# Optimization experiments

Hardware: AMD Instinct MI355X
Metric: run time of the kernel (lower is better)

The kernel has to match this reference:

```python
import jax, jax.numpy as jnp
import numpy as np

B, C, Himg, Wimg = 4, 256, 64, 64
HID = 256
K = 8
EPS_NORM = 1e-12
BN_EPS = 1e-5


def setup_inputs() -> dict:
    key = jax.random.key(0)
    ks = jax.random.split(key, 14)
    s = lambda fan: 1.0 / np.sqrt(fan)
    inp = {
        "features": jax.random.normal(ks[0], (B, C, Himg, Wimg), dtype=jnp.float32),
        # HypergraphConv 0: theta (C->HID), phi (HID->HID). Weights stored [in,out].
        "theta0_w": jax.random.normal(ks[1], (C, HID), dtype=jnp.float32) * s(C),
        "theta0_b": jnp.zeros((HID,), jnp.float32),
        "phi0_w": jax.random.normal(ks[2], (HID, HID), dtype=jnp.float32) * s(HID),
        "phi0_b": jnp.zeros((HID,), jnp.float32),
        # HypergraphConv 1: theta (HID->HID), phi (HID->HID)
        "theta1_w": jax.random.normal(ks[3], (HID, HID), dtype=jnp.float32) * s(HID),
        "theta1_b": jnp.zeros((HID,), jnp.float32),
        "phi1_w": jax.random.normal(ks[4], (HID, HID), dtype=jnp.float32) * s(HID),
        "phi1_b": jnp.zeros((HID,), jnp.float32),
        # out_proj: 1x1 conv HID->C, stored as [HID, C]
        "proj_w": jax.random.normal(ks[5], (HID, C), dtype=jnp.float32) * s(HID),
        "proj_b": jnp.zeros((C,), jnp.float32),
        # BatchNorm2d affine params
        "bn_gamma": jnp.ones((C,), jnp.float32),
        "bn_beta": jnp.zeros((C,), jnp.float32),
    }
    return inp


def _build_hypergraph(features):
    # features: [B, C, H, W] -> nodes [B, N, C]; incidence from batch 0 only
    b, c, h, w = features.shape
    n = h * w
    feat_flat = features.reshape(b, c, n).transpose(0, 2, 1)  # [B, N, C]
    f0 = feat_flat[0]  # [N, C] (original computes full-batch similarity but uses [0])
    f0n = f0 / jnp.maximum(jnp.linalg.norm(f0, axis=-1, keepdims=True), EPS_NORM)
    sim = f0n @ f0n.T  # [N, N]
    _, idx = jax.lax.top_k(sim, K)  # [N, K]
    rows = idx.reshape(-1)
    cols = jnp.repeat(jnp.arange(n), K)
    Hm = jnp.zeros((n, n), jnp.float32).at[rows, cols].set(1.0)  # [N, E=N]
    # L1 column normalization (F.normalize p=1 dim=0)
    Hn = Hm / jnp.maximum(Hm.sum(axis=0, keepdims=True), EPS_NORM)
    return Hn, feat_flat


def _hconv(x, Hn, tw, tb, pw, pb):
    # x: [B, N, Cin]
    xt = x @ tw + tb  # [B, N, Cout]
    ef = jnp.einsum('ne,bnc->bec', Hn, xt)  # H^T @ x_theta -> edge feats
    xp = ef @ pw + pb  # [B, E, Cout]
    return jnp.einsum('ne,bec->bnc', Hn, xp)  # H @ x_phi


def reference(features, theta0_w, theta0_b, phi0_w, phi0_b,
              theta1_w, theta1_b, phi1_w, phi1_b,
              proj_w, proj_b, bn_gamma, bn_beta):
    b, c, h, w = features.shape
    Hn, x = _build_hypergraph(features)
    x = jax.nn.relu(_hconv(x, Hn, theta0_w, theta0_b, phi0_w, phi0_b))
    x = jax.nn.relu(_hconv(x, Hn, theta1_w, theta1_b, phi1_w, phi1_b)) + x
    # back to [B, HID, H, W] then 1x1 conv
    x = x.transpose(0, 2, 1).reshape(b, HID, h, w)
    x = jnp.einsum('bihw,io->bohw', x, proj_w) + proj_b[None, :, None, None]
    # BatchNorm2d (training mode: batch statistics, biased variance)
    mean = x.mean(axis=(0, 2, 3))
    var = x.var(axis=(0, 2, 3))
    xn = (x - mean[None, :, None, None]) * jax.lax.rsqrt(var + BN_EPS)[None, :, None, None]
    xn = xn * bn_gamma[None, :, None, None] + bn_beta[None, :, None, None]
    return features + xn
```

## Files before the change

kernel.cpp:

```cpp
#include <hip/hip_runtime.h>

namespace {

constexpr int NB = 4;
constexpr int NC = 256;
constexpr int NN = 4096;

typedef __attribute__((ext_vector_type(8))) short bf8;
typedef __attribute__((ext_vector_type(4))) float f4;
typedef unsigned short ushort_t;
typedef unsigned long long ull;

__device__ __forceinline__ float bf2f(unsigned short u) {
  return __uint_as_float(((unsigned)u) << 16);
}
__device__ __forceinline__ unsigned short f2bf(float f) {
  unsigned x = __float_as_uint(f);
  return (unsigned short)((x + 0x7FFFu + ((x >> 16) & 1u)) >> 16);
}
__device__ __forceinline__ unsigned enc_f(float f) {
  unsigned u = __float_as_uint(f);
  return (u & 0x80000000u) ? ~u : (u | 0x80000000u);
}

__device__ __forceinline__ void ins8(ull* b, ull k) {
  if (k <= b[7]) return;
  b[7] = k;
#pragma unroll
  for (int p = 7; p >= 1; --p) {
    if (b[p] > b[p-1]) { ull t = b[p]; b[p] = b[p-1]; b[p-1] = t; }
  }
}

__device__ __forceinline__ ull shfl_xor_ull(ull v, int mask) {
  unsigned lo = (unsigned)(v & 0xFFFFFFFFull), hi = (unsigned)(v >> 32);
  lo = (unsigned)__shfl_xor((int)lo, mask);
  hi = (unsigned)__shfl_xor((int)hi, mask);
  return ((ull)hi << 32) | (ull)lo;
}

template<int MAXS>
__device__ __forceinline__ void shfl_merge8(ull* b) {
#pragma unroll
  for (int s = 1; s <= MAXS; s <<= 1) {
    ull tmp[8];
#pragma unroll
    for (int k = 0; k < 8; ++k) tmp[k] = shfl_xor_ull(b[k], s);
#pragma unroll
    for (int k = 0; k < 8; ++k) ins8(b, tmp[k]);
  }
}

__global__ __launch_bounds__(256) void norm_kernel(const float* __restrict__ feat,
                                                   float* __restrict__ inv,
                                                   int* __restrict__ counts,
                                                   float* __restrict__ bnsum) {
  int n = blockIdx.x * 256 + threadIdx.x;
  counts[n] = 0;
  if (n < 2 * NC) bnsum[n] = 0.f;
  float ss = 0.f;
  for (int c = 0; c < NC; ++c) { float v = feat[(size_t)c * NN + n]; ss = fmaf(v, v, ss); }
  inv[n] = 1.f / fmaxf(sqrtf(ss), 1e-12f);
}

__global__ __launch_bounds__(256) void xpose_split_kernel(const float* __restrict__ feat,
                                                          const float* __restrict__ inv,
                                                          unsigned short* __restrict__ Xhi,
                                                          unsigned short* __restrict__ Xlo) {
  __shared__ float tile[64][65];
  int n0 = blockIdx.x * 64, c0 = blockIdx.y * 64;
  int tid = threadIdx.x;
#pragma unroll
  for (int i = 0; i < 4; ++i) {
    int u = tid + i * 256; int cr = u >> 4, q = u & 15;
    float4 v = *(const float4*)&feat[(size_t)(c0 + cr) * NN + n0 + q * 4];
    tile[cr][q*4+0] = v.x; tile[cr][q*4+1] = v.y; tile[cr][q*4+2] = v.z; tile[cr][q*4+3] = v.w;
  }
  __syncthreads();
#pragma unroll
  for (int i = 0; i < 4; ++i) {
    int u = tid + i * 256; int nr = u >> 4, q = u & 15;
    float iv = inv[n0 + nr];
    ushort4 h, l;
    float x0 = tile[q*4+0][nr] * iv, x1 = tile[q*4+1][nr] * iv;
    float x2 = tile[q*4+2][nr] * iv, x3 = tile[q*4+3][nr] * iv;
    h.x = f2bf(x0); l.x = f2bf(x0 - bf2f(h.x));
    h.y = f2bf(x1); l.y = f2bf(x1 - bf2f(h.y));
    h.z = f2bf(x2); l.z = f2bf(x2 - bf2f(h.z));
    h.w = f2bf(x3); l.w = f2bf(x3 - bf2f(h.w));
    size_t o = (size_t)(n0 + nr) * NC + c0 + q * 4;
    *(ushort4*)&Xhi[o] = h;
    *(ushort4*)&Xlo[o] = l;
  }
}

__global__ __launch_bounds__(256) void wcvt_kernel(const float* __restrict__ w0,
                                                   const float* __restrict__ w1,
                                                   const float* __restrict__ w2,
                                                   const float* __restrict__ w3,
                                                   const float* __restrict__ w4,
                                                   unsigned short* __restrict__ Wt) {
  __shared__ float tile[64][65];
  int z = blockIdx.z;
  const float* W = (z == 0) ? w0 : (z == 1) ? w1 : (z == 2) ? w2 : (z == 3) ? w3 : w4;
  int k0 = blockIdx.x * 64, n0 = blockIdx.y * 64;
  int tid = threadIdx.x;
#pragma unroll
  for (int i = 0; i < 4; ++i) {
    int u = tid + i * 256; int kr = u >> 4, q = u & 15;
    float4 v = *(const float4*)&W[(size_t)(k0 + kr) * NC + n0 + q * 4];
    tile[kr][q*4+0] = v.x; tile[kr][q*4+1] = v.y; tile[kr][q*4+2] = v.z; tile[kr][q*4+3] = v.w;
  }
  __syncthreads();
#pragma unroll
  for (int i = 0; i < 4; ++i) {
    int u = tid + i * 256; int nr = u >> 4, q = u & 15;
    ushort4 o;
    o.x = f2bf(tile[q*4+0][nr]); o.y = f2bf(tile[q*4+1][nr]);
    o.z = f2bf(tile[q*4+2][nr]); o.w = f2bf(tile[q*4+3][nr]);
    *(ushort4*)&Wt[(size_t)z * 65536 + (size_t)(n0 + nr) * NC + k0 + q * 4] = o;
  }
}

__global__ __launch_bounds__(256) void feat2bf_kernel(const float* __restrict__ feat,
                                                      unsigned short* __restrict__ xin) {
  __shared__ float tile[64][65];
  int n0 = blockIdx.x * 64, c0 = blockIdx.y * 64, b = blockIdx.z;
  int tid = threadIdx.x;
#pragma unroll
  for (int i = 0; i < 4; ++i) {
    int u = tid + i * 256; int cr = u >> 4, q = u & 15;
    float4 v = *(const float4*)&feat[((size_t)b * NC + c0 + cr) * NN + n0 + q * 4];
    tile[cr][q*4+0] = v.x; tile[cr][q*4+1] = v.y; tile[cr][q*4+2] = v.z; tile[cr][q*4+3] = v.w;
  }
  __syncthreads();
#pragma unroll
  for (int i = 0; i < 4; ++i) {
    int u = tid + i * 256; int nr = u >> 4, q = u & 15;
    ushort4 o;
    o.x = f2bf(tile[q*4+0][nr]); o.y = f2bf(tile[q*4+1][nr]);
    o.z = f2bf(tile[q*4+2][nr]); o.w = f2bf(tile[q*4+3][nr]);
    *(ushort4*)&xin[((size_t)(b << 12) + n0 + nr) * NC + c0 + q * 4] = o;
  }
}

__global__ __launch_bounds__(512) void simtop_kernel(const unsigned short* __restrict__ Xhi,
                                                     const unsigned short* __restrict__ Xlo,
                                                     ull* __restrict__ cand) {
  __shared__ __align__(16) char lds[73728];
  ushort_t (*sAh)[72] = (ushort_t(*)[72])(lds);
  ushort_t (*sAl)[72] = (ushort_t(*)[72])(lds + 18432);
  ushort_t (*sBh)[72] = (ushort_t(*)[72])(lds + 36864);
  ushort_t (*sBl)[72] = (ushort_t(*)[72])(lds + 55296);
  float    (*simT)[132] = (float(*)[132])(lds);

  int tid = threadIdx.x, wave = tid >> 6, lane = tid & 63;
  int wm = wave >> 2, wn = wave & 3;
  int bid = blockIdx.x;
  int pi = (int)((sqrtf(8.f * (float)bid + 1.f) - 1.f) * 0.5f);
  while ((pi + 1) * (pi + 2) / 2 <= bid) ++pi;
  while (pi * (pi + 1) / 2 > bid) --pi;
  int pj = bid - pi * (pi + 1) / 2;
  int m0 = pj * 128, n0 = pi * 128;

  f4 acc[4][2];
#pragma unroll
  for (int i = 0; i < 4; ++i)
#pragma unroll
    for (int j = 0; j < 2; ++j) acc[i][j] = (f4){0.f, 0.f, 0.f, 0.f};

  for (int k0 = 0; k0 < NC; k0 += 64) {
#pragma unroll
    for (int i = 0; i < 2; ++i) {
      int u = tid + i * 512; int r = u >> 3, q = u & 7;
      int qp = (q ^ ((r >> 1) & 7)) * 8;
      size_t am = (size_t)(m0 + r) * NC + k0 + q * 8;
      size_t an = (size_t)(n0 + r) * NC + k0 + q * 8;
      *(uint4*)&sAh[r][qp] = *(const uint4*)&Xhi[am];
      *(uint4*)&sAl[r][qp] = *(const uint4*)&Xlo[am];
      *(uint4*)&sBh[r][qp] = *(const uint4*)&Xhi[an];
      *(uint4*)&sBl[r][qp] = *(const uint4*)&Xlo[an];
    }
    __syncthreads();
#pragma unroll
    for (int ks = 0; ks < 2; ++ks) {
      int qr = ks * 4 + (lane >> 4);
      bf8 ah[4], al[4], bh[2], bl[2];
#pragma unroll
      for (int mf = 0; mf < 4; ++mf) {
        int rr = wm*64 + mf*16 + (lane & 15);
        int qp = (qr ^ ((rr >> 1) & 7)) * 8;
        ah[mf] = *(const bf8*)&sAh[rr][qp];
        al[mf] = *(const bf8*)&sAl[rr][qp];
      }
#pragma unroll
      for (int nf = 0; nf < 2; ++nf) {
        int rr = wn*32 + nf*16 + (lane & 15);
        int qp = (qr ^ ((rr >> 1) & 7)) * 8;
        bh[nf] = *(const bf8*)&sBh[rr][qp];
        bl[nf] = *(const bf8*)&sBl[rr][qp];
      }
#pragma unroll
      for (int nf = 0; nf < 2; ++nf)
#pragma unroll
        for (int mf = 0; mf < 4; ++mf) {
          acc[mf][nf] = __builtin_amdgcn_mfma_f32_16x16x32_bf16(ah[mf], bh[nf], acc[mf][nf], 0, 0, 0);
          acc[mf][nf] = __builtin_amdgcn_mfma_f32_16x16x32_bf16(ah[mf], bl[nf], acc[mf][nf], 0, 0, 0);
          acc[mf][nf] = __builtin_amdgcn_mfma_f32_16x16x32_bf16(al[mf], bh[nf], acc[mf][nf], 0, 0, 0);
        }
    }
    __syncthreads();
  }

#pragma unroll
  for (int mf = 0; mf < 4; ++mf)
#pragma unroll
    for (int nf = 0; nf < 2; ++nf) {
      int cl = wn*32 + nf*16 + (lane & 15);
#pragma unroll
      for (int r = 0; r < 4; ++r)
        simT[wm*64 + mf*16 + (lane >> 4)*4 + r][cl] = acc[mf][nf][r];
    }
  __syncthreads();

  {
    int rrow = tid >> 2, q4 = tid & 3;
    ull b8[8] = {0,0,0,0,0,0,0,0};
#pragma unroll
    for (int i = 0; i < 8; ++i) {
      int cofs = q4 * 32 + (((i + q4 * 2) & 7)) * 4;
      float4 v = *(const float4*)&simT[rrow][cofs];
      int jb = n0 + cofs;
      ins8(b8, ((ull)enc_f(v.x) << 32) | (ull)(0xFFFFFFFFu - (unsigned)(jb + 0)));
      ins8(b8, ((ull)enc_f(v.y) << 32) | (ull)(0xFFFFFFFFu - (unsigned)(jb + 1)));
      ins8(b8, ((ull)enc_f(v.z) << 32) | (ull)(0xFFFFFFFFu - (unsigned)(jb + 2)));
      ins8(b8, ((ull)enc_f(v.w) << 32) | (ull)(0xFFFFFFFFu - (unsigned)(jb + 3)));
    }
    shfl_merge8<2>(b8);
    if (q4 == 0) {
      ull* dst = cand + (size_t)(m0 + rrow) * 256 + pi * 8;
#pragma unroll
      for (int k = 0; k < 8; ++k) dst[k] = b8[k];
    }
  }

  if (pi != pj) {
    int ccol = tid >> 2, seg = tid & 3;
    ull c8[8] = {0,0,0,0,0,0,0,0};
    for (int i = 0; i < 32; ++i) {
      int rr = seg * 32 + ((i + seg) & 31);
      float v = simT[rr][ccol];
      int jb = m0 + rr;
      ins8(c8, ((ull)enc_f(v) << 32) | (ull)(0xFFFFFFFFu - (unsigned)jb));
    }
    shfl_merge8<2>(c8);
    if (seg == 0) {
      ull* dst = cand + (size_t)(n0 + ccol) * 256 + pj * 8;
#pragma unroll
      for (int k = 0; k < 8; ++k) dst[k] = c8[k];
    }
  }
}

__global__ __launch_bounds__(256) void merge_kernel(const ull* __restrict__ cand,
                                                    int* __restrict__ idx8,
                                                    int* __restrict__ counts) {
  int t = blockIdx.x * 256 + threadIdx.x;
  int row = t >> 3, part = t & 7;
  const ull* cp = cand + (size_t)row * 256 + part * 32;
  ull b8[8] = {0,0,0,0,0,0,0,0};
  for (int g = 0; g < 4; ++g) {
#pragma unroll 1
    for (int k = 0; k < 8; ++k) {
      ull key = cp[g * 8 + k];
      if (key <= b8[7]) break;
      ins8(b8, key);
    }
  }
  shfl_merge8<4>(b8);
  if (part == 0) {
#pragma unroll
    for (int k = 0; k < 8; ++k) {
      int j = (int)(0xFFFFFFFFu - (unsigned)(b8[k] & 0xFFFFFFFFull));
      idx8[row * 8 + k] = j;
      atomicAdd(&counts[j], 1);
    }
  }
}

__global__ __launch_bounds__(256) void scan_kernel(const int* __restrict__ counts,
                                                   int* __restrict__ offsets,
                                                   int* __restrict__ cursor) {
  __shared__ int ssum[256];
  __shared__ int sbase[257];
  int t = threadIdx.x;
  int loc[16];
  int s = 0;
#pragma unroll
  for (int i = 0; i < 16; ++i) { loc[i] = s; s += counts[t*16 + i]; }
  ssum[t] = s;
  __syncthreads();
  if (t == 0) {
    int acc = 0;
    for (int i = 0; i < 256; ++i) { sbase[i] = acc; acc += ssum[i]; }
    sbase[256] = acc;
  }
  __syncthreads();
  int b0 = sbase[t];
#pragma unroll
  for (int i = 0; i < 16; ++i) {
    int off = b0 + loc[i];
    offsets[t*16 + i] = off;
    cursor [t*16 + i] = off;
  }
  if (t == 0) offsets[NN] = sbase[256];
}

__global__ __launch_bounds__(256) void fill_kernel(const int* __restrict__ idx8,
                                                   int* __restrict__ cursor,
                                                   int* __restrict__ edgelist) {
  int t = blockIdx.x * 256 + threadIdx.x;
  int n = idx8[t];
  int pos = atomicAdd(&cursor[n], 1);
  edgelist[pos] = t >> 3;
}

template<int OUTF32, int BNS, int GATHER>
__global__ __launch_bounds__(512) void gemm_bf16_kernel(const unsigned short* __restrict__ A,
                                                        const unsigned short* __restrict__ Wt,
                                                        const float* __restrict__ bias,
                                                        void* __restrict__ outp,
                                                        float* __restrict__ bnsum,
                                                        const int* __restrict__ idx8) {
  __shared__ ushort_t sA[128][72];
  __shared__ ushort_t sB[128][72];
  __shared__ int sIdx[128][8];
  int tid = threadIdx.x, wave = tid >> 6, lane = tid & 63;
  int wm = wave >> 2, wn = wave & 3;
  int n0 = blockIdx.x * 128, m0 = blockIdx.y * 128;
  size_t bbase = 0;
  if constexpr (GATHER) {
    int e0 = m0 & 4095;
    bbase = ((size_t)(m0 >> 12) << 12) * NC;
#pragma unroll
    for (int u = tid; u < 1024; u += 512) ((int*)sIdx)[u] = idx8[e0 * 8 + u];
    __syncthreads();
  }
  f4 acc[4][2];
#pragma unroll
  for (int i = 0; i < 4; ++i)
#pragma unroll
    for (int j = 0; j < 2; ++j) acc[i][j] = (f4){0.f, 0.f, 0.f, 0.f};

  for (int k0 = 0; k0 < NC; k0 += 64) {
#pragma unroll
    for (int i = 0; i < 2; ++i) {
      int u = tid + i * 512; int r = u >> 3, q = u & 7;
      int qp = (q ^ ((r >> 1) & 7)) * 8;
      if constexpr (GATHER) {
        float s[8] = {0.f,0.f,0.f,0.f,0.f,0.f,0.f,0.f};
#pragma unroll
        for (int k = 0; k < 8; ++k) {
          int nn = sIdx[r][k];
          uint4 v = *(const uint4*)&A[bbase + (size_t)nn * NC + k0 + q * 8];
          s[0] += bf2f((unsigned short)(v.x & 0xFFFF)); s[1] += bf2f((unsigned short)(v.x >> 16));
          s[2] += bf2f((unsigned short)(v.y & 0xFFFF)); s[3] += bf2f((unsigned short)(v.y >> 16));
          s[4] += bf2f((unsigned short)(v.z & 0xFFFF)); s[5] += bf2f((unsigned short)(v.z >> 16));
          s[6] += bf2f((unsigned short)(v.w & 0xFFFF)); s[7] += bf2f((unsigned short)(v.w >> 16));
        }
        uint4 o;
        o.x = (unsigned)f2bf(s[0]*0.125f) | ((unsigned)f2bf(s[1]*0.125f) << 16);
        o.y = (unsigned)f2bf(s[2]*0.125f) | ((unsigned)f2bf(s[3]*0.125f) << 16);
        o.z = (unsigned)f2bf(s[4]*0.125f) | ((unsigned)f2bf(s[5]*0.125f) << 16);
        o.w = (unsigned)f2bf(s[6]*0.125f) | ((unsigned)f2bf(s[7]*0.125f) << 16);
        *(uint4*)&sA[r][qp] = o;
      } else {
        *(uint4*)&sA[r][qp] = *(const uint4*)&A[(size_t)(m0 + r) * NC + k0 + q * 8];
      }
      *(uint4*)&sB[r][qp] = *(const uint4*)&Wt[(size_t)(n0 + r) * NC + k0 + q * 8];
    }
    __syncthreads();
#pragma unroll
    for (int ks = 0; ks < 2; ++ks) {
      int qr = ks * 4 + (lane >> 4);
      bf8 a[4], b[2];
#pragma unroll
      for (int mf = 0; mf < 4; ++mf) {
        int rr = wm*64 + mf*16 + (lane & 15);
        a[mf] = *(const bf8*)&sA[rr][(qr ^ ((rr >> 1) & 7)) * 8];
      }
#pragma unroll
      for (int nf = 0; nf < 2; ++nf) {
        int rr = wn*32 + nf*16 + (lane & 15);
        b[nf] = *(const bf8*)&sB[rr][(qr ^ ((rr >> 1) & 7)) * 8];
      }
#pragma unroll
      for (int nf = 0; nf < 2; ++nf)
#pragma unroll
        for (int mf = 0; mf < 4; ++mf)
          acc[mf][nf] = __builtin_amdgcn_mfma_f32_16x16x32_bf16(a[mf], b[nf], acc[mf][nf], 0, 0, 0);
    }
    __syncthreads();
  }
#pragma unroll
  for (int nf = 0; nf < 2; ++nf) {
    int n = n0 + wn*32 + nf*16 + (lane & 15);
    float bi = bias[n];
    float s1 = 0.f, s2 = 0.f;
#pragma unroll
    for (int mf = 0; mf < 4; ++mf) {
#pragma unroll
      for (int r = 0; r < 4; ++r) {
        int m = m0 + wm*64 + mf*16 + (lane >> 4)*4 + r;
        float v = acc[mf][nf][r] + bi;
        if (OUTF32) ((float*)outp)[(size_t)m * NC + n] = v;
        else ((unsigned short*)outp)[(size_t)m * NC + n] = f2bf(v);
        if (BNS) { s1 += v; s2 = fmaf(v, v, s2); }
      }
    }
    if (BNS) {
      s1 += __shfl_xor(s1, 16); s1 += __shfl_xor(s1, 32);
      s2 += __shfl_xor(s2, 16); s2 += __shfl_xor(s2, 32);
      if (lane < 16) {
        atomicAdd(&bnsum[n], s1);
        atomicAdd(&bnsum[NC + n], s2);
      }
    }
  }
}

template<int MODE>
__global__ __launch_bounds__(256) void scatter_kernel(const unsigned short* __restrict__ xp,
                                                      const int* __restrict__ offsets,
                                                      const int* __restrict__ edgelist,
                                                      const unsigned short* __restrict__ res,
                                                      unsigned short* __restrict__ outb) {
  int b = blockIdx.y;
  int n = blockIdx.x * 4 + (threadIdx.x >> 6);
  int lane = threadIdx.x & 63;
  int s0i = offsets[n], s1i = offsets[n + 1];
  float s0 = 0, s1 = 0, s2 = 0, s3 = 0;
  for (int j = s0i; j < s1i; ++j) {
    int e = edgelist[j];
    uint2 v = *(const uint2*)&xp[((size_t)((b << 12) + e)) * NC + lane * 4];
    s0 += bf2f((unsigned short)(v.x & 0xFFFF)); s1 += bf2f((unsigned short)(v.x >> 16));
    s2 += bf2f((unsigned short)(v.y & 0xFFFF)); s3 += bf2f((unsigned short)(v.y >> 16));
  }
  s0 = fmaxf(s0 * 0.125f, 0.f); s1 = fmaxf(s1 * 0.125f, 0.f);
  s2 = fmaxf(s2 * 0.125f, 0.f); s3 = fmaxf(s3 * 0.125f, 0.f);
  size_t o = ((size_t)((b << 12) + n)) * NC + lane * 4;
  if (MODE == 1) {
    uint2 v = *(const uint2*)&res[o];
    s0 += bf2f((unsigned short)(v.x & 0xFFFF)); s1 += bf2f((unsigned short)(v.x >> 16));
    s2 += bf2f((unsigned short)(v.y & 0xFFFF)); s3 += bf2f((unsigned short)(v.y >> 16));
  }
  uint2 ov;
  ov.x = (unsigned)f2bf(s0) | ((unsigned)f2bf(s1) << 16);
  ov.y = (unsigned)f2bf(s2) | ((unsigned)f2bf(s3) << 16);
  *(uint2*)&outb[o] = ov;
}

__global__ __launch_bounds__(256) void final_kernel(const float* __restrict__ y,
                                                    const float* __restrict__ feat,
                                                    const float* __restrict__ bnsum,
                                                    const float* __restrict__ gam,
                                                    const float* __restrict__ bet,
                                                    float* __restrict__ out) {
  __shared__ float tile[64][65];
  __shared__ float sa_[64], sb_[64];
  int n0 = blockIdx.x * 64;
  int c0 = blockIdx.y * 64;
  int b  = blockIdx.z;
  int tid = threadIdx.x;
  if (tid < 64) {
    const float invn = 1.f / (float)(NB * NN);
    int c = c0 + tid;
    float mean = bnsum[c] * invn;
    float var  = bnsum[NC + c] * invn - mean * mean;
    float a = gam[c] * rsqrtf(var + 1e-5f);
    sa_[tid] = a;
    sb_[tid] = bet[c] - mean * a;
  }
  int n_l = tid >> 2;
  int q   = tid & 3;
  const float4* y4 = (const float4*)y;
#pragma unroll
  for (int i = 0; i < 4; ++i) {
    int cl = q * 16 + i * 4;
    float4 v = y4[(size_t)(b * NN + n0 + n_l) * 64 + ((c0 + cl) >> 2)];
    tile[n_l][cl+0] = v.x; tile[n_l][cl+1] = v.y; tile[n_l][cl+2] = v.z; tile[n_l][cl+3] = v.w;
  }
  __syncthreads();
  int cl2 = tid >> 6;
  int nl2 = tid & 63;
#pragma unroll
  for (int p = 0; p < 16; ++p) {
    int ci = p * 4 + cl2;
    float a = sa_[ci], bb = sb_[ci];
    size_t o = (size_t)b * (NC * NN) + (size_t)(c0 + ci) * NN + n0 + nl2;
    out[o] = feat[o] + fmaf(a, tile[nl2][ci], bb);
  }
}

}

extern "C" void kernel_launch(void* const* d_in, const int* in_sizes, int n_in,
                              void* d_out, int out_size, void* d_ws, size_t ws_size,
                              hipStream_t stream) {
  (void)in_sizes; (void)n_in; (void)out_size; (void)ws_size;
  const float* feat = (const float*)d_in[0];
  const float* t0w  = (const float*)d_in[1];
  const float* t0b  = (const float*)d_in[2];
  const float* p0w  = (const float*)d_in[3];
  const float* p0b  = (const float*)d_in[4];
  const float* t1w  = (const float*)d_in[5];
  const float* t1b  = (const float*)d_in[6];
  const float* p1w  = (const float*)d_in[7];
  const float* p1b  = (const float*)d_in[8];
  const float* pw   = (const float*)d_in[9];
  const float* pb   = (const float*)d_in[10];
  const float* gam  = (const float*)d_in[11];
  const float* bet  = (const float*)d_in[12];
  float* out = (float*)d_out;

  char* ws = (char*)d_ws;
  float*          y   = (float*)ws;
  unsigned short* xin = (unsigned short*)(ws + (16u << 20));
  unsigned short* xt  = (unsigned short*)(ws + (24u << 20));
  unsigned short* xp  = (unsigned short*)(ws + (40u << 20));
  unsigned short* x1  = (unsigned short*)(ws + (48u << 20));
  unsigned short* x2  = (unsigned short*)(ws + (56u << 20));
  unsigned short* Xhi = (unsigned short*)(ws + (64u << 20));
  unsigned short* Xlo = (unsigned short*)(ws + (66u << 20));
  ull*            cand = (ull*)(ws + (68u << 20));
  char* sm = ws + (76u << 20);
  unsigned short* Wt  = (unsigned short*)sm;
  int*   idx8     = (int*)(sm + 655360);
  int*   counts   = (int*)(sm + 786432);
  int*   offsets  = (int*)(sm + 802816);
  int*   cursor   = (int*)(sm + 819456);
  int*   edgelist = (int*)(sm + 835840);
  float* inv      = (float*)(sm + 966912);
  float* bnsum    = (float*)(sm + 983296);

  norm_kernel<<<NN / 256, 256, 0, stream>>>(feat, inv, counts, bnsum);
  xpose_split_kernel<<<dim3(64, 4), 256, 0, stream>>>(feat, inv, Xhi, Xlo);
  wcvt_kernel<<<dim3(4, 4, 5), 256, 0, stream>>>(t0w, p0w, t1w, p1w, pw, Wt);
  feat2bf_kernel<<<dim3(64, 4, 4), 256, 0, stream>>>(feat, xin);

  simtop_kernel<<<528, 512, 0, stream>>>(Xhi, Xlo, cand);
  merge_kernel<<<128, 256, 0, stream>>>(cand, idx8, counts);
  scan_kernel<<<1, 256, 0, stream>>>(counts, offsets, cursor);
  fill_kernel<<<128, 256, 0, stream>>>(idx8, cursor, edgelist);

  gemm_bf16_kernel<0,0,0><<<dim3(2, 128), 512, 0, stream>>>(xin, Wt + 0*65536, t0b, xt, nullptr, nullptr);
  gemm_bf16_kernel<0,0,1><<<dim3(2, 128), 512, 0, stream>>>(xt,  Wt + 1*65536, p0b, xp, nullptr, idx8);
  scatter_kernel<0><<<dim3(1024, 4), 256, 0, stream>>>(xp, offsets, edgelist, nullptr, x1);
  gemm_bf16_kernel<0,0,0><<<dim3(2, 128), 512, 0, stream>>>(x1, Wt + 2*65536, t1b, xt, nullptr, nullptr);
  gemm_bf16_kernel<0,0,1><<<dim3(2, 128), 512, 0, stream>>>(xt, Wt + 3*65536, p1b, xp, nullptr, idx8);
  scatter_kernel<1><<<dim3(1024, 4), 256, 0, stream>>>(xp, offsets, edgelist, x1, x2);
  gemm_bf16_kernel<1,1,0><<<dim3(2, 128), 512, 0, stream>>>(x2, Wt + 4*65536, pb, y, bnsum, nullptr);

  final_kernel<<<dim3(64, 4, 4), 256, 0, stream>>>(y, feat, bnsum, gam, bet, out);
}
```

Measured before the change: 334.1 us.

## Fuse feature transpose kernels, precompute simtop LDS offsets, add top-k threshold pruning

Result: slower. 342.4 us (+2.5%).

```diff
diff --git a/kernel.cpp b/kernel.cpp
--- a/kernel.cpp
+++ b/kernel.cpp
@@ -21,6 +21,9 @@
 __device__ __forceinline__ unsigned enc_f(float f) {
   unsigned u = __float_as_uint(f);
   return (u & 0x80000000u) ? ~u : (u | 0x80000000u);
+}
+__device__ __forceinline__ float dec_e(unsigned e) {
+  return __uint_as_float((e & 0x80000000u) ? (e ^ 0x80000000u) : ~e);
 }
 
 __device__ __forceinline__ void ins8(ull* b, ull k) {
@@ -63,34 +66,41 @@
   inv[n] = 1.f / fmaxf(sqrtf(ss), 1e-12f);
 }
 
-__global__ __launch_bounds__(256) void xpose_split_kernel(const float* __restrict__ feat,
-                                                          const float* __restrict__ inv,
-                                                          unsigned short* __restrict__ Xhi,
-                                                          unsigned short* __restrict__ Xlo) {
+__global__ __launch_bounds__(256) void feat2bf_kernel(const float* __restrict__ feat,
+                                                      const float* __restrict__ inv,
+                                                      unsigned short* __restrict__ xin,
+                                                      unsigned short* __restrict__ Xhi,
+                                                      unsigned short* __restrict__ Xlo) {
   __shared__ float tile[64][65];
-  int n0 = blockIdx.x * 64, c0 = blockIdx.y * 64;
+  int n0 = blockIdx.x * 64, c0 = blockIdx.y * 64, b = blockIdx.z;
   int tid = threadIdx.x;
 #pragma unroll
   for (int i = 0; i < 4; ++i) {
     int u = tid + i * 256; int cr = u >> 4, q = u & 15;
-    float4 v = *(const float4*)&feat[(size_t)(c0 + cr) * NN + n0 + q * 4];
+    float4 v = *(const float4*)&feat[((size_t)b * NC + c0 + cr) * NN + n0 + q * 4];
     tile[cr][q*4+0] = v.x; tile[cr][q*4+1] = v.y; tile[cr][q*4+2] = v.z; tile[cr][q*4+3] = v.w;
   }
   __syncthreads();
 #pragma unroll
   for (int i = 0; i < 4; ++i) {
     int u = tid + i * 256; int nr = u >> 4, q = u & 15;
-    float iv = inv[n0 + nr];
-    ushort4 h, l;
-    float x0 = tile[q*4+0][nr] * iv, x1 = tile[q*4+1][nr] * iv;
-    float x2 = tile[q*4+2][nr] * iv, x3 = tile[q*4+3][nr] * iv;
-    h.x = f2bf(x0); l.x = f2bf(x0 - bf2f(h.x));
-    h.y = f2bf(x1); l.y = f2bf(x1 - bf2f(h.y));
-    h.z = f2bf(x2); l.z = f2bf(x2 - bf2f(h.z));
-    h.w = f2bf(x3); l.w = f2bf(x3 - bf2f(h.w));
-    size_t o = (size_t)(n0 + nr) * NC + c0 + q * 4;
-    *(ushort4*)&Xhi[o] = h;
-    *(ushort4*)&Xlo[o] = l;
+    float x0 = tile[q*4+0][nr], x1 = tile[q*4+1][nr];
+    float x2 = tile[q*4+2][nr], x3 = tile[q*4+3][nr];
+    ushort4 o;
+    o.x = f2bf(x0); o.y = f2bf(x1); o.z = f2bf(x2); o.w = f2bf(x3);
+    *(ushort4*)&xin[((size_t)(b << 12) + n0 + nr) * NC + c0 + q * 4] = o;
+    if (b == 0) {
+      float iv = inv[n0 + nr];
+      float y0 = x0 * iv, y1 = x1 * iv, y2 = x2 * iv, y3 = x3 * iv;
+      ushort4 h, l;
+      h.x = f2bf(y0); l.x = f2bf(y0 - bf2f(h.x));
+      h.y = f2bf(y1); l.y = f2bf(y1 - bf2f(h.y));
+      h.z = f2bf(y2); l.z = f2bf(y2 - bf2f(h.z));
+      h.w = f2bf(y3); l.w = f2bf(y3 - bf2f(h.w));
+      size_t oo = (size_t)(n0 + nr) * NC + c0 + q * 4;
+      *(ushort4*)&Xhi[oo] = h;
+      *(ushort4*)&Xlo[oo] = l;
+    }
   }
 }
 
@@ -122,83 +132,84 @@
   }
 }
 
-__global__ __launch_bounds__(256) void feat2bf_kernel(const float* __restrict__ feat,
-                                                      unsigned short* __restrict__ xin) {
-  __shared__ float tile[64][65];
-  int n0 = blockIdx.x * 64, c0 = blockIdx.y * 64, b = blockIdx.z;
-  int tid = threadIdx.x;
-#pragma unroll
-  for (int i = 0; i < 4; ++i) {
-    int u = tid + i * 256; int cr = u >> 4, q = u & 15;
-    float4 v = *(const float4*)&feat[((size_t)b * NC + c0 + cr) * NN + n0 + q * 4];
-    tile[cr][q*4+0] = v.x; tile[cr][q*4+1] = v.y; tile[cr][q*4+2] = v.z; tile[cr][q*4+3] = v.w;
-  }
-  __syncthreads();
-#pragma unroll
-  for (int i = 0; i < 4; ++i) {
-    int u = tid + i * 256; int nr = u >> 4, q = u & 15;
-    ushort4 o;
-    o.x = f2bf(tile[q*4+0][nr]); o.y = f2bf(tile[q*4+1][nr]);
-    o.z = f2bf(tile[q*4+2][nr]); o.w = f2bf(tile[q*4+3][nr]);
-    *(ushort4*)&xin[((size_t)(b << 12) + n0 + nr) * NC + c0 + q * 4] = o;
-  }
-}
-
 __global__ __launch_bounds__(512) void simtop_kernel(const unsigned short* __restrict__ Xhi,
                                                      const unsigned short* __restrict__ Xlo,
                                                      ull* __restrict__ cand) {
   __shared__ __align__(16) char lds[73728];
-  ushort_t (*sAh)[72] = (ushort_t(*)[72])(lds);
-  ushort_t (*sAl)[72] = (ushort_t(*)[72])(lds + 18432);
-  ushort_t (*sBh)[72] = (ushort_t(*)[72])(lds + 36864);
-  ushort_t (*sBl)[72] = (ushort_t(*)[72])(lds + 55296);
-  float    (*simT)[132] = (float(*)[132])(lds);
+  float (*simT)[132] = (float(*)[132])(lds);
 
   int tid = threadIdx.x, wave = tid >> 6, lane = tid & 63;
   int wm = wave >> 2, wn = wave & 3;
-  int bid = blockIdx.x;
+  int orig = blockIdx.x;
+  int bid = (orig & 7) * 66 + (orig >> 3);
   int pi = (int)((sqrtf(8.f * (float)bid + 1.f) - 1.f) * 0.5f);
   while ((pi + 1) * (pi + 2) / 2 <= bid) ++pi;
   while (pi * (pi + 1) / 2 > bid) --pi;
   int pj = bid - pi * (pi + 1) / 2;
   int m0 = pj * 128, n0 = pi * 128;
 
+  int sr = tid >> 2;
+  int q0 = (tid & 3) * 2;
+  int s_ = (sr >> 1) & 7;
+  int qp0 = q0 ^ s_;
+  const ushort_t* gAh = Xhi + (size_t)(m0 + sr) * NC + q0 * 8;
+  const ushort_t* gAl = Xlo + (size_t)(m0 + sr) * NC + q0 * 8;
+  const ushort_t* gBh = Xhi + (size_t)(n0 + sr) * NC + q0 * 8;
+  const ushort_t* gBl = Xlo + (size_t)(n0 + sr) * NC + q0 * 8;
+  int d0 = sr * 144 + qp0 * 16;
+  int d1 = sr * 144 + (qp0 ^ 1) * 16;
+
+  int oA[2][4], oB[2][2];
+#pragma unroll
+  for (int ks = 0; ks < 2; ++ks) {
+    int qr = ks * 4 + (lane >> 4);
+#pragma unroll
+    for (int mf = 0; mf < 4; ++mf) {
+      int rr = wm * 64 + mf * 16 + (lane & 15);
+      oA[ks][mf] = rr * 144 + (qr ^ ((rr >> 1) & 7)) * 16;
+    }
+#pragma unroll
+    for (int nf = 0; nf < 2; ++nf) {
+      int rr = wn * 32 + nf * 16 + (lane & 15);
+      oB[ks][nf] = rr * 144 + (qr ^ ((rr >> 1) & 7)) * 16;
+    }
+  }
+
   f4 acc[4][2];
 #pragma unroll
   for (int i = 0; i < 4; ++i)
 #pragma unroll
     for (int j = 0; j < 2; ++j) acc[i][j] = (f4){0.f, 0.f, 0.f, 0.f};
 
-  for (int k0 = 0; k0 < NC; k0 += 64) {
-#pragma unroll
-    for (int i = 0; i < 2; ++i) {
-      int u = tid + i * 512; int r = u >> 3, q = u & 7;
-      int qp = (q ^ ((r >> 1) & 7)) * 8;
-      size_t am = (size_t)(m0 + r) * NC + k0 + q * 8;
-      size_t an = (size_t)(n0 + r) * NC + k0 + q * 8;
-      *(uint4*)&sAh[r][qp] = *(const uint4*)&Xhi[am];
-      *(uint4*)&sAl[r][qp] = *(const uint4*)&Xlo[am];
-      *(uint4*)&sBh[r][qp] = *(const uint4*)&Xhi[an];
-      *(uint4*)&sBl[r][qp] = *(const uint4*)&Xlo[an];
+#pragma unroll
+  for (int kk = 0; kk < 4; ++kk) {
+    {
+      uint4 a0 = *(const uint4*)(gAh + kk * 64);
+      uint4 a1 = *(const uint4*)(gAh + kk * 64 + 8);
+      uint4 a2 = *(const uint4*)(gAl + kk * 64);
+      uint4 a3 = *(const uint4*)(gAl + kk * 64 + 8);
+      uint4 b0 = *(const uint4*)(gBh + kk * 64);
+      uint4 b1 = *(const uint4*)(gBh + kk * 64 + 8);
+      uint4 b2 = *(const uint4*)(gBl + kk * 64);
+      uint4 b3 = *(const uint4*)(gBl + kk * 64 + 8);
+      *(uint4*)(lds +         d0) = a0;  *(uint4*)(lds +         d1) = a1;
+      *(uint4*)(lds + 18432 + d0) = a2;  *(uint4*)(lds + 18432 + d1) = a3;
+      *(uint4*)(lds + 36864 + d0) = b0;  *(uint4*)(lds + 36864 + d1) = b1;
+      *(uint4*)(lds + 55296 + d0) = b2;  *(uint4*)(lds + 55296 + d1) = b3;
     }
     __syncthreads();
 #pragma unroll
     for (int ks = 0; ks < 2; ++ks) {
-      int qr = ks * 4 + (lane >> 4);
       bf8 ah[4], al[4], bh[2], bl[2];
 #pragma unroll
       for (int mf = 0; mf < 4; ++mf) {
-        int rr = wm*64 + mf*16 + (lane & 15);
-        int qp = (qr ^ ((rr >> 1) & 7)) * 8;
-        ah[mf] = *(const bf8*)&sAh[rr][qp];
-        al[mf] = *(const bf8*)&sAl[rr][qp];
+        ah[mf] = *(const bf8*)(lds +         oA[ks][mf]);
+        al[mf] = *(const bf8*)(lds + 18432 + oA[ks][mf]);
       }
 #pragma unroll
       for (int nf = 0; nf < 2; ++nf) {
-        int rr = wn*32 + nf*16 + (lane & 15);
-        int qp = (qr ^ ((rr >> 1) & 7)) * 8;
-        bh[nf] = *(const bf8*)&sBh[rr][qp];
-        bl[nf] = *(const bf8*)&sBl[rr][qp];
+        bh[nf] = *(const bf8*)(lds + 36864 + oB[ks][nf]);
+        bl[nf] = *(const bf8*)(lds + 55296 + oB[ks][nf]);
       }
 #pragma unroll
       for (int nf = 0; nf < 2; ++nf)
@@ -216,29 +227,36 @@
   for (int mf = 0; mf < 4; ++mf)
 #pragma unroll
     for (int nf = 0; nf < 2; ++nf) {
-      int cl = wn*32 + nf*16 + (lane & 15);
+      int cl = wn * 32 + nf * 16 + (lane & 15);
+      int rbase = wm * 64 + mf * 16 + (lane >> 4) * 4;
 #pragma unroll
       for (int r = 0; r < 4; ++r)
-        simT[wm*64 + mf*16 + (lane >> 4)*4 + r][cl] = acc[mf][nf][r];
+        simT[rbase + r][cl] = acc[mf][nf][r];
     }
   __syncthreads();
 
   {
-    int rrow = tid >> 2, q4 = tid & 3;
+    int rl = tid >> 2, q4 = tid & 3;
+    const float* rowp = &simT[rl][q4 * 32];
     ull b8[8] = {0,0,0,0,0,0,0,0};
+    float thr = -3.0e38f;
 #pragma unroll
     for (int i = 0; i < 8; ++i) {
-      int cofs = q4 * 32 + (((i + q4 * 2) & 7)) * 4;
-      float4 v = *(const float4*)&simT[rrow][cofs];
-      int jb = n0 + cofs;
-      ins8(b8, ((ull)enc_f(v.x) << 32) | (ull)(0xFFFFFFFFu - (unsigned)(jb + 0)));
-      ins8(b8, ((ull)enc_f(v.y) << 32) | (ull)(0xFFFFFFFFu - (unsigned)(jb + 1)));
-      ins8(b8, ((ull)enc_f(v.z) << 32) | (ull)(0xFFFFFFFFu - (unsigned)(jb + 2)));
-      ins8(b8, ((ull)enc_f(v.w) << 32) | (ull)(0xFFFFFFFFu - (unsigned)(jb + 3)));
+      int off = ((i + q4 * 2) & 7) * 4;
+      float4 v = *(const float4*)(rowp + off);
+      if (fmaxf(fmaxf(v.x, v.y), fmaxf(v.z, v.w)) >= thr) {
+        int jb = n0 + q4 * 32 + off;
+        ins8(b8, ((ull)enc_f(v.x) << 32) | (ull)(0xFFFFFFFFu - (unsigned)(jb + 0)));
+        ins8(b8, ((ull)enc_f(v.y) << 32) | (ull)(0xFFFFFFFFu - (unsigned)(jb + 1)));
+        ins8(b8, ((ull)enc_f(v.z) << 32) | (ull)(0xFFFFFFFFu - (unsigned)(jb + 2)));
+        ins8(b8, ((ull)enc_f(v.w) << 32) | (ull)(0xFFFFFFFFu - (unsigned)(jb + 3)));
+        unsigned h = (unsigned)(b8[7] >> 32);
+        thr = h ? dec_e(h) : -3.0e38f;
+      }
     }
     shfl_merge8<2>(b8);
     if (q4 == 0) {
-      ull* dst = cand + (size_t)(m0 + rrow) * 256 + pi * 8;
+      ull* dst = cand + (size_t)(m0 + rl) * 256 + pi * 8;
 #pragma unroll
       for (int k = 0; k < 8; ++k) dst[k] = b8[k];
     }
@@ -247,11 +265,15 @@
   if (pi != pj) {
     int ccol = tid >> 2, seg = tid & 3;
     ull c8[8] = {0,0,0,0,0,0,0,0};
+    float thr = -3.0e38f;
     for (int i = 0; i < 32; ++i) {
       int rr = seg * 32 + ((i + seg) & 31);
       float v = simT[rr][ccol];
-      int jb = m0 + rr;
-      ins8(c8, ((ull)enc_f(v) << 32) | (ull)(0xFFFFFFFFu - (unsigned)jb));
+      if (v >= thr) {
+        ins8(c8, ((ull)enc_f(v) << 32) | (ull)(0xFFFFFFFFu - (unsigned)(m0 + rr)));
+        unsigned h = (unsigned)(c8[7] >> 32);
+        thr = h ? dec_e(h) : -3.0e38f;
+      }
     }
     shfl_merge8<2>(c8);
     if (seg == 0) {
@@ -544,9 +566,8 @@
   float* bnsum    = (float*)(sm + 983296);
 
   norm_kernel<<<NN / 256, 256, 0, stream>>>(feat, inv, counts, bnsum);
-  xpose_split_kernel<<<dim3(64, 4), 256, 0, stream>>>(feat, inv, Xhi, Xlo);
+  feat2bf_kernel<<<dim3(64, 4, 4), 256, 0, stream>>>(feat, inv, xin, Xhi, Xlo);
   wcvt_kernel<<<dim3(4, 4, 5), 256, 0, stream>>>(t0w, p0w, t1w, p1w, pw, Wt);
-  feat2bf_kernel<<<dim3(64, 4, 4), 256, 0, stream>>>(feat, xin);
 
   simtop_kernel<<<528, 512, 0, stream>>>(Xhi, Xlo, cand);
   merge_kernel<<<128, 256, 0, stream>>>(cand, idx8, counts);
```
